# Performance work log

Measured on AMD Instinct MI355X. Metric: run time of the kernel, lower is better.

Reference implementation:

```python
import math
import jax, jax.numpy as jnp
import numpy as np

INPUT_DIM = 512
HIDDEN_DIM = 512
BATCH = 8
SEQ_LEN = 4096


def _xavier(key, shape):
    fan_out, fan_in = shape
    limit = math.sqrt(6.0 / (fan_in + fan_out))
    return jax.random.uniform(key, shape, jnp.float32, -limit, limit)


def setup_inputs() -> dict:
    key = jax.random.key(0)
    kx, kA, kB, kC, kD, kWg = jax.random.split(key, 6)
    return {
        "x": jax.random.normal(kx, (BATCH, SEQ_LEN, INPUT_DIM), jnp.float32),
        "A": jax.random.uniform(kA, (HIDDEN_DIM,), jnp.float32, 0.8, 0.95),
        "B": _xavier(kB, (HIDDEN_DIM, INPUT_DIM)),
        "C": _xavier(kC, (HIDDEN_DIM, HIDDEN_DIM)),
        "D": _xavier(kD, (HIDDEN_DIM, INPUT_DIM)),
        "Wg": _xavier(kWg, (HIDDEN_DIM, INPUT_DIM)),
        "bias_h": jnp.zeros((HIDDEN_DIM,), jnp.float32),
        "bias_y": jnp.zeros((HIDDEN_DIM,), jnp.float32),
    }


def reference(x, A, B, C, D, Wg, bias_h, bias_y):
    # x: (b, t, i). Eval mode: dropout is identity.
    hidden_dim = A.shape[0]
    # Precompute all input-dependent per-step terms as batched GEMMs.
    g = jnp.clip(jax.nn.sigmoid(jnp.einsum('bti,hi->bth', x, Wg)), 0.05, 0.95)
    xB = jnp.einsum('bti,hi->bth', x, B)
    # h_t = h_{t-1} + g_t*(A*h_{t-1} + xB_t + bias_h - h_{t-1})
    #     = (1 - g_t*(1 - A)) * h_{t-1} + g_t*(xB_t + bias_h)
    a_coef = 1.0 - g * (1.0 - A)          # (b, t, h)
    b_coef = g * (xB + bias_h)            # (b, t, h)

    def step(h, ab):
        a_t, b_t = ab
        h = a_t * h + b_t
        return h, h

    h0 = jnp.zeros((x.shape[0], hidden_dim), x.dtype)
    _, hs = jax.lax.scan(step, h0, (jnp.swapaxes(a_coef, 0, 1), jnp.swapaxes(b_coef, 0, 1)))
    hs = jnp.swapaxes(hs, 0, 1)           # (b, t, h)

    scale = 1.0 / math.sqrt(hidden_dim)
    y = (jnp.einsum('bth,oh->bto', hs, C) + jnp.einsum('bti,hi->bth', x, D) + bias_y) * scale
    return y
```

## Files before the change

### kernel.cpp

```cpp
#include <hip/hip_runtime.h>
#include <math.h>

#define MTOT 32768
#define KD 512
#define HD 512
#define NB 8
#define TS 4096
#define NCHUNK 64
#define TCHUNK 64

typedef __attribute__((ext_vector_type(8))) short bf16x8;
typedef __attribute__((ext_vector_type(4))) float f32x4;
typedef __attribute__((ext_vector_type(4))) unsigned short us4;

#define GLD16(gsrc, ldst) __builtin_amdgcn_global_load_lds( \
    (const __attribute__((address_space(1))) void*)(gsrc),   \
    (__attribute__((address_space(3))) void*)(ldst), 16, 0, 0)

__device__ __forceinline__ unsigned short f2bf(float f) {
    unsigned u = __float_as_uint(f);
    return (unsigned short)((u + 0x7FFFu + ((u >> 16) & 1u)) >> 16);
}
__device__ __forceinline__ float bf2f(unsigned short u) {
    return __uint_as_float(((unsigned)u) << 16);
}

__global__ __launch_bounds__(256) void cast_all(
    const float* __restrict__ x, const float* __restrict__ B,
    const float* __restrict__ G, const float* __restrict__ C,
    const float* __restrict__ D,
    unsigned short* __restrict__ x16, unsigned short* __restrict__ w16)
{
    const int blk = blockIdx.x;
    const float* src;
    unsigned short* dst;
    int i;
    if (blk < (MTOT * KD / 1024)) {
        src = x; dst = x16;
        i = blk * 1024 + threadIdx.x * 4;
    } else {
        const int r = blk - (MTOT * KD / 1024);
        const int mat = r >> 8;
        src = (mat == 0) ? B : (mat == 1) ? G : (mat == 2) ? C : D;
        dst = w16 + (size_t)mat * (HD * KD);
        i = (r & 255) * 1024 + threadIdx.x * 4;
    }
    float4 v = *(const float4*)(src + i);
    us4 o; o.x = f2bf(v.x); o.y = f2bf(v.y); o.z = f2bf(v.z); o.w = f2bf(v.w);
    *(us4*)(dst + i) = o;
}

__global__ __launch_bounds__(256, 4) void in_gemm_mfma(
    const short* __restrict__ xb, const short* __restrict__ wmat,
    const float* __restrict__ Avec, const float* __restrict__ bias_h,
    unsigned* __restrict__ ab16, float2* __restrict__ chPS)
{
    __shared__ __align__(16) short Xs[2][128 * 32];
    __shared__ __align__(16) short Ws[2][2][64 * 32];
    const int tid = threadIdx.x;
    const int w = tid >> 6, l = tid & 63;
    const int bid = blockIdx.x;
    const int xcd = bid & 7;
    const int jj  = bid >> 3;
    const int n0  = (jj & 7) * 64;
    const int m0  = (xcd * 32 + (jj >> 3)) * 128;
    const int wm = (w & 1) * 64;
    const int wn = (w >> 1) * 32;

    int xsrc[2], xdst[2];
    #pragma unroll
    for (int j = 0; j < 2; ++j) {
        const int s = (w * 2 + j) * 64 + l;
        const int r = s >> 2, gg = (s & 3) ^ ((r >> 1) & 3);
        xsrc[j] = (m0 + r) * KD + gg * 8;
        xdst[j] = s * 8;
    }
    int wsrc, wdsts;
    {
        const int s = w * 64 + l;
        const int r = s >> 2, gg = (s & 3) ^ ((r >> 1) & 3);
        wsrc = (n0 + r) * KD + gg * 8;
        wdsts = s * 8;
    }

#define STAGE_IN(TI, BUF) do {                                              \
    const int kk_ = (TI) * 32;                                              \
    _Pragma("unroll")                                                       \
    for (int j_ = 0; j_ < 2; ++j_)                                          \
        GLD16(xb + xsrc[j_] + kk_, &Xs[BUF][xdst[j_]]);                     \
    _Pragma("unroll")                                                       \
    for (int m_ = 0; m_ < 2; ++m_)                                          \
        GLD16(wmat + (size_t)m_ * (HD * KD) + wsrc + kk_,                   \
              &Ws[BUF][m_][wdsts]);                                         \
} while (0)

    f32x4 acc[2][4][2];
    #pragma unroll
    for (int a = 0; a < 2; ++a)
        #pragma unroll
        for (int i = 0; i < 4; ++i)
            #pragma unroll
            for (int j = 0; j < 2; ++j) acc[a][i][j] = (f32x4)0.0f;

    STAGE_IN(0, 0);
    STAGE_IN(1, 1);

    const int g = l >> 4;
    #pragma unroll
    for (int it = 0; it < 16; ++it) {
        const int cur = it & 1;
        if (it < 15) asm volatile("s_waitcnt vmcnt(4)" ::: "memory");
        else         asm volatile("s_waitcnt vmcnt(0)" ::: "memory");
        __builtin_amdgcn_s_barrier();
        __builtin_amdgcn_s_setprio(1);
        bf16x8 af[4];
        #pragma unroll
        for (int mt = 0; mt < 4; ++mt) {
            const int r = wm + mt * 16 + (l & 15);
            const int sg = g ^ ((r >> 1) & 3);
            af[mt] = *(const bf16x8*)(&Xs[cur][r * 32 + sg * 8]);
        }
        #pragma unroll
        for (int mat = 0; mat < 2; ++mat) {
            #pragma unroll
            for (int nt = 0; nt < 2; ++nt) {
                const int r = wn + nt * 16 + (l & 15);
                const int sg = g ^ ((r >> 1) & 3);
                bf16x8 bfv = *(const bf16x8*)(&Ws[cur][mat][r * 32 + sg * 8]);
                #pragma unroll
                for (int mt = 0; mt < 4; ++mt)
                    acc[mat][mt][nt] = __builtin_amdgcn_mfma_f32_16x16x32_bf16(
                        af[mt], bfv, acc[mat][mt][nt], 0, 0, 0);
            }
        }
        __builtin_amdgcn_s_setprio(0);
        asm volatile("s_waitcnt lgkmcnt(0)" ::: "memory");
        __builtin_amdgcn_s_barrier();
        if (it < 14) STAGE_IN(it + 2, cur);
    }
#undef STAGE_IN

    const int q  = l >> 4;
    const int cl = l & 15;
    const int bidx   = m0 >> 12;
    const int c_in_b = ((m0 & (TS - 1)) >> 6) + (w & 1);
    #pragma unroll
    for (int nt = 0; nt < 2; ++nt) {
        const int n = n0 + wn + nt * 16 + cl;
        const float An1 = 1.0f - Avec[n];
        const float bh  = bias_h[n];
        float Pc = 1.0f, Sc = 0.0f;
        #pragma unroll
        for (int mt = 0; mt < 4; ++mt) {
            float Pl = 1.0f, Sl = 0.0f;
            #pragma unroll
            for (int r = 0; r < 4; ++r) {
                const float vB = acc[0][mt][nt][r];
                const float vG = acc[1][mt][nt][r];
                float g2 = __builtin_amdgcn_rcpf(1.0f + __expf(-vG));
                g2 = fminf(fmaxf(g2, 0.05f), 0.95f);
                const unsigned short su = f2bf(g2 * An1);
                const unsigned short bu = f2bf(g2 * (vB + bh));
                const float a  = 1.0f - bf2f(su);
                const float bb = bf2f(bu);
                const int m = m0 + wm + mt * 16 + q * 4 + r;
                ab16[(size_t)m * HD + n] = (unsigned)su | ((unsigned)bu << 16);
                Sl = fmaf(a, Sl, bb);
                Pl *= a;
            }
            float Pm = 1.0f, Sm = 0.0f;
            #pragma unroll
            for (int k = 0; k < 4; ++k) {
                const float Pk = __shfl(Pl, cl + 16 * k, 64);
                const float Sk = __shfl(Sl, cl + 16 * k, 64);
                Sm = fmaf(Pk, Sm, Sk);
                Pm *= Pk;
            }
            Sc = fmaf(Pm, Sc, Sm);
            Pc *= Pm;
        }
        if (q == 0) {
            chPS[(size_t)c_in_b * (NB * HD) + bidx * HD + n] = make_float2(Pc, Sc);
        }
    }
}

__global__ __launch_bounds__(256) void scan_pass3(
    const unsigned* __restrict__ ab, const float2* __restrict__ chPS,
    unsigned short* __restrict__ hs_out)
{
    const int g = blockIdx.x * blockDim.x + threadIdx.x;
    const int h = g & (HD - 1);
    const int rest = g >> 9;
    const int b = rest & (NB - 1);
    const int c = rest >> 3;
    const float2* p = chPS + (size_t)b * HD + h;
    float hv = 0.0f;
    for (int j = 0; j < c; ++j) {
        const float2 ps = p[(size_t)j * (NB * HD)];
        hv = fmaf(ps.x, hv, ps.y);
    }
    size_t idx = ((size_t)(b * TS + c * TCHUNK)) * HD + h;
    #pragma unroll 4
    for (int t = 0; t < TCHUNK; ++t) {
        const unsigned v = ab[idx];
        const float a  = 1.0f - bf2f((unsigned short)(v & 0xFFFFu));
        const float bb = bf2f((unsigned short)(v >> 16));
        hv = fmaf(a, hv, bb);
        hs_out[idx] = f2bf(hv);
        idx += HD;
    }
}

__global__ __launch_bounds__(256, 2) void out_gemm_dual(
    const short* __restrict__ hs, const short* __restrict__ xb,
    const short* __restrict__ Cb, const short* __restrict__ Db,
    const float* __restrict__ bias_y, float* __restrict__ y)
{
    __shared__ __align__(16) short Hs[128 * 64];
    __shared__ __align__(16) short Xs2[128 * 64];
    __shared__ __align__(16) short Cs[128 * 64];
    __shared__ __align__(16) short Ds[128 * 64];
    const int tid = threadIdx.x;
    const int w = tid >> 6, l = tid & 63;
    const int m0 = blockIdx.x * 128;
    const int n0 = blockIdx.y * 128;
    const int wm = (w & 1) * 64;
    const int wn = (w >> 1) * 64;

    int src_m[4], src_n[4], dst_s[4];
    #pragma unroll
    for (int j = 0; j < 4; ++j) {
        const int s = (w * 4 + j) * 64 + l;
        const int r = s >> 3, g = (s & 7) ^ (r & 7);
        src_m[j] = (m0 + r) * HD + g * 8;
        src_n[j] = (n0 + r) * HD + g * 8;
        dst_s[j] = (w * 4 + j) * 64 * 8;
    }

    f32x4 acc[4][4];
    #pragma unroll
    for (int i = 0; i < 4; ++i)
        #pragma unroll
        for (int j = 0; j < 4; ++j) acc[i][j] = (f32x4)0.0f;

    for (int kk = 0; kk < HD; kk += 64) {
        __syncthreads();
        #pragma unroll
        for (int j = 0; j < 4; ++j) {
            GLD16(hs + src_m[j] + kk, Hs  + dst_s[j]);
            GLD16(xb + src_m[j] + kk, Xs2 + dst_s[j]);
            GLD16(Cb + src_n[j] + kk, Cs  + dst_s[j]);
            GLD16(Db + src_n[j] + kk, Ds  + dst_s[j]);
        }
        __syncthreads();
        #pragma unroll
        for (int kc = 0; kc < 2; ++kc) {
            const int g = kc * 4 + (l >> 4);
            {
                bf16x8 af[4], bfv[4];
                #pragma unroll
                for (int t = 0; t < 4; ++t) {
                    const int ra = wm + t * 16 + (l & 15);
                    af[t] = *(const bf16x8*)(Hs + ra * 64 + ((g ^ (ra & 7)) * 8));
                    const int rb = wn + t * 16 + (l & 15);
                    bfv[t] = *(const bf16x8*)(Cs + rb * 64 + ((g ^ (rb & 7)) * 8));
                }
                #pragma unroll
                for (int mt = 0; mt < 4; ++mt)
                    #pragma unroll
                    for (int nt = 0; nt < 4; ++nt)
                        acc[mt][nt] = __builtin_amdgcn_mfma_f32_16x16x32_bf16(
                            af[mt], bfv[nt], acc[mt][nt], 0, 0, 0);
            }
            {
                bf16x8 af[4], bfv[4];
                #pragma unroll
                for (int t = 0; t < 4; ++t) {
                    const int ra = wm + t * 16 + (l & 15);
                    af[t] = *(const bf16x8*)(Xs2 + ra * 64 + ((g ^ (ra & 7)) * 8));
                    const int rb = wn + t * 16 + (l & 15);
                    bfv[t] = *(const bf16x8*)(Ds + rb * 64 + ((g ^ (rb & 7)) * 8));
                }
                #pragma unroll
                for (int mt = 0; mt < 4; ++mt)
                    #pragma unroll
                    for (int nt = 0; nt < 4; ++nt)
                        acc[mt][nt] = __builtin_amdgcn_mfma_f32_16x16x32_bf16(
                            af[mt], bfv[nt], acc[mt][nt], 0, 0, 0);
            }
        }
    }

    const float scale = 0.04419417382415922f;
    #pragma unroll
    for (int nt = 0; nt < 4; ++nt) {
        const int n = n0 + wn + nt * 16 + (l & 15);
        const float by = bias_y[n];
        #pragma unroll
        for (int mt = 0; mt < 4; ++mt) {
            #pragma unroll
            for (int r = 0; r < 4; ++r) {
                const int m = m0 + wm + mt * 16 + (l >> 4) * 4 + r;
                y[(size_t)m * HD + n] = (acc[mt][nt][r] + by) * scale;
            }
        }
    }
}

extern "C" void kernel_launch(void* const* d_in, const int* in_sizes, int n_in,
                              void* d_out, int out_size, void* d_ws, size_t ws_size,
                              hipStream_t stream) {
    const float* x      = (const float*)d_in[0];
    const float* Avec   = (const float*)d_in[1];
    const float* Bw     = (const float*)d_in[2];
    const float* Cw     = (const float*)d_in[3];
    const float* Dw     = (const float*)d_in[4];
    const float* Wg     = (const float*)d_in[5];
    const float* bias_h = (const float*)d_in[6];
    const float* bias_y = (const float*)d_in[7];
    float* y = (float*)d_out;

    unsigned* ab16        = (unsigned*)d_ws;
    unsigned short* x16   = (unsigned short*)(ab16 + (size_t)MTOT * HD);
    unsigned short* hs16  = x16 + (size_t)MTOT * HD;
    unsigned short* w16   = hs16 + (size_t)MTOT * HD;
    float2* chPS = (float2*)(w16 + (size_t)4 * HD * KD);

    cast_all<<<MTOT * KD / 1024 + 4 * (HD * KD / 1024), 256, 0, stream>>>(
        x, Bw, Wg, Cw, Dw, x16, w16);

    in_gemm_mfma<<<2048, 256, 0, stream>>>(
        (const short*)x16, (const short*)w16, Avec, bias_h, ab16, chPS);

    scan_pass3<<<(NB * HD * NCHUNK) / 256, 256, 0, stream>>>(ab16, chPS, hs16);

    out_gemm_dual<<<dim3(MTOT / 128, HD / 128), 256, 0, stream>>>(
        (const short*)hs16, (const short*)x16,
        (const short*)(w16 + (size_t)2 * HD * KD),
        (const short*)(w16 + (size_t)3 * HD * KD), bias_y, y);
}
```

Before: 252.9 us.

## Double-buffer output GEMM LDS tiles with async global-to-LDS prefetch

Restructures the output dual-GEMM main loop from single-buffered 64-wide K tiles into double-buffered 32-wide K tiles. Each stage's global-to-LDS loads are issued two iterations ahead and waited on with explicit vmcnt counts, so memory transfer overlaps MFMA compute. The swizzle is adapted to 32-element rows, and s_setprio is raised around the MFMA section. It adds more barriers per K step and depends on hand-tuned waitcnt values being correct.

```diff
diff --git a/kernel.cpp b/kernel.cpp
--- a/kernel.cpp
+++ b/kernel.cpp
@@ -217,10 +217,10 @@
     const short* __restrict__ Cb, const short* __restrict__ Db,
     const float* __restrict__ bias_y, float* __restrict__ y)
 {
-    __shared__ __align__(16) short Hs[128 * 64];
-    __shared__ __align__(16) short Xs2[128 * 64];
-    __shared__ __align__(16) short Cs[128 * 64];
-    __shared__ __align__(16) short Ds[128 * 64];
+    __shared__ __align__(16) short Hs[2][128 * 32];
+    __shared__ __align__(16) short Xs2[2][128 * 32];
+    __shared__ __align__(16) short Cs[2][128 * 32];
+    __shared__ __align__(16) short Ds[2][128 * 32];
     const int tid = threadIdx.x;
     const int w = tid >> 6, l = tid & 63;
     const int m0 = blockIdx.x * 128;
@@ -228,15 +228,26 @@
     const int wm = (w & 1) * 64;
     const int wn = (w >> 1) * 64;
 
-    int src_m[4], src_n[4], dst_s[4];
-    #pragma unroll
-    for (int j = 0; j < 4; ++j) {
-        const int s = (w * 4 + j) * 64 + l;
-        const int r = s >> 3, g = (s & 7) ^ (r & 7);
-        src_m[j] = (m0 + r) * HD + g * 8;
-        src_n[j] = (n0 + r) * HD + g * 8;
-        dst_s[j] = (w * 4 + j) * 64 * 8;
-    }
+    int src_m[2], src_n[2], dst_s[2];
+    #pragma unroll
+    for (int j = 0; j < 2; ++j) {
+        const int s = (w * 2 + j) * 64 + l;
+        const int r = s >> 2, gg = (s & 3) ^ ((r >> 1) & 3);
+        src_m[j] = (m0 + r) * HD + gg * 8;
+        src_n[j] = (n0 + r) * HD + gg * 8;
+        dst_s[j] = s * 8;
+    }
+
+#define STAGE_OUT(TI, BUF) do {                                         \
+    const int kk_ = (TI) * 32;                                          \
+    _Pragma("unroll")                                                   \
+    for (int j_ = 0; j_ < 2; ++j_) {                                    \
+        GLD16(hs + src_m[j_] + kk_, &Hs [BUF][dst_s[j_]]);              \
+        GLD16(xb + src_m[j_] + kk_, &Xs2[BUF][dst_s[j_]]);              \
+        GLD16(Cb + src_n[j_] + kk_, &Cs [BUF][dst_s[j_]]);              \
+        GLD16(Db + src_n[j_] + kk_, &Ds [BUF][dst_s[j_]]);              \
+    }                                                                   \
+} while (0)
 
     f32x4 acc[4][4];
     #pragma unroll
@@ -244,53 +255,59 @@
         #pragma unroll
         for (int j = 0; j < 4; ++j) acc[i][j] = (f32x4)0.0f;
 
-    for (int kk = 0; kk < HD; kk += 64) {
-        __syncthreads();
-        #pragma unroll
-        for (int j = 0; j < 4; ++j) {
-            GLD16(hs + src_m[j] + kk, Hs  + dst_s[j]);
-            GLD16(xb + src_m[j] + kk, Xs2 + dst_s[j]);
-            GLD16(Cb + src_n[j] + kk, Cs  + dst_s[j]);
-            GLD16(Db + src_n[j] + kk, Ds  + dst_s[j]);
-        }
-        __syncthreads();
-        #pragma unroll
-        for (int kc = 0; kc < 2; ++kc) {
-            const int g = kc * 4 + (l >> 4);
-            {
-                bf16x8 af[4], bfv[4];
+    STAGE_OUT(0, 0);
+    STAGE_OUT(1, 1);
+
+    const int g = l >> 4;
+    #pragma unroll
+    for (int ti = 0; ti < 16; ++ti) {
+        const int cur = ti & 1;
+        if (ti < 15) asm volatile("s_waitcnt vmcnt(8)" ::: "memory");
+        else         asm volatile("s_waitcnt vmcnt(0)" ::: "memory");
+        __builtin_amdgcn_s_barrier();
+        __builtin_amdgcn_s_setprio(1);
+        {
+            bf16x8 af[4], bfv[4];
+            #pragma unroll
+            for (int t = 0; t < 4; ++t) {
+                const int ra = wm + t * 16 + (l & 15);
+                const int sa = g ^ ((ra >> 1) & 3);
+                af[t] = *(const bf16x8*)(&Hs[cur][ra * 32 + sa * 8]);
+                const int rb = wn + t * 16 + (l & 15);
+                const int sb = g ^ ((rb >> 1) & 3);
+                bfv[t] = *(const bf16x8*)(&Cs[cur][rb * 32 + sb * 8]);
+            }
+            #pragma unroll
+            for (int mt = 0; mt < 4; ++mt)
                 #pragma unroll
-                for (int t = 0; t < 4; ++t) {
-                    const int ra = wm + t * 16 + (l & 15);
-                    af[t] = *(const bf16x8*)(Hs + ra * 64 + ((g ^ (ra & 7)) * 8));
-                    const int rb = wn + t * 16 + (l & 15);
-                    bfv[t] = *(const bf16x8*)(Cs + rb * 64 + ((g ^ (rb & 7)) * 8));
-                }
+                for (int nt = 0; nt < 4; ++nt)
+                    acc[mt][nt] = __builtin_amdgcn_mfma_f32_16x16x32_bf16(
+                        af[mt], bfv[nt], acc[mt][nt], 0, 0, 0);
+        }
+        {
+            bf16x8 af[4], bfv[4];
+            #pragma unroll
+            for (int t = 0; t < 4; ++t) {
+                const int ra = wm + t * 16 + (l & 15);
+                const int sa = g ^ ((ra >> 1) & 3);
+                af[t] = *(const bf16x8*)(&Xs2[cur][ra * 32 + sa * 8]);
+                const int rb = wn + t * 16 + (l & 15);
+                const int sb = g ^ ((rb >> 1) & 3);
+                bfv[t] = *(const bf16x8*)(&Ds[cur][rb * 32 + sb * 8]);
+            }
+            #pragma unroll
+            for (int mt = 0; mt < 4; ++mt)
                 #pragma unroll
-                for (int mt = 0; mt < 4; ++mt)
-                    #pragma unroll
-                    for (int nt = 0; nt < 4; ++nt)
-                        acc[mt][nt] = __builtin_amdgcn_mfma_f32_16x16x32_bf16(
-                            af[mt], bfv[nt], acc[mt][nt], 0, 0, 0);
-            }
-            {
-                bf16x8 af[4], bfv[4];
-                #pragma unroll
-                for (int t = 0; t < 4; ++t) {
-                    const int ra = wm + t * 16 + (l & 15);
-                    af[t] = *(const bf16x8*)(Xs2 + ra * 64 + ((g ^ (ra & 7)) * 8));
-                    const int rb = wn + t * 16 + (l & 15);
-                    bfv[t] = *(const bf16x8*)(Ds + rb * 64 + ((g ^ (rb & 7)) * 8));
-                }
-                #pragma unroll
-                for (int mt = 0; mt < 4; ++mt)
-                    #pragma unroll
-                    for (int nt = 0; nt < 4; ++nt)
-                        acc[mt][nt] = __builtin_amdgcn_mfma_f32_16x16x32_bf16(
-                            af[mt], bfv[nt], acc[mt][nt], 0, 0, 0);
-            }
-        }
-    }
+                for (int nt = 0; nt < 4; ++nt)
+                    acc[mt][nt] = __builtin_amdgcn_mfma_f32_16x16x32_bf16(
+                        af[mt], bfv[nt], acc[mt][nt], 0, 0, 0);
+        }
+        __builtin_amdgcn_s_setprio(0);
+        asm volatile("s_waitcnt lgkmcnt(0)" ::: "memory");
+        __builtin_amdgcn_s_barrier();
+        if (ti < 14) STAGE_OUT(ti + 2, cur);
+    }
+#undef STAGE_OUT
 
     const float scale = 0.04419417382415922f;
     #pragma unroll
```

Measured after the change: 254.2 us. Within noise of the previous version (+0.5%).
